# Kernel tuning notes

Measured on AMD Instinct MI355X. Metric: run time of the kernel, lower is better.

The kernel has to match this reference:

```python
import jax, jax.numpy as jnp
import numpy as np

NIN = 4096
NOUT = 4096
LN_EPS = 1e-5  # torch.nn.LayerNorm default


def setup_inputs() -> dict:
    key = jax.random.key(0)
    ks = jax.random.split(key, 8)
    x = jax.random.normal(ks[0], (1, NIN), dtype=jnp.float32)
    hid = jax.random.normal(ks[1], (1, NOUT), dtype=jnp.float32)
    hebb = jnp.zeros((NOUT, NOUT), dtype=jnp.float32) + 1e-6  # initialZeroHebb
    # parameters
    w_in = 0.01 * jax.random.normal(ks[2], (NOUT, NIN), dtype=jnp.float32)  # inp_lin weight (no bias)
    w = 0.01 * jnp.eye(NOUT, NOUT, dtype=jnp.float32)                        # Plastic.w
    alpha = 0.01 * jax.random.normal(ks[3], (NOUT, NOUT), dtype=jnp.float32)
    b = 0.01 * jax.random.normal(ks[4], (NOUT,), dtype=jnp.float32)
    lamda = 0.01 * jnp.ones((1,), dtype=jnp.float32)
    pred_eta = 0.01 * jax.random.normal(ks[5], (NOUT, NOUT), dtype=jnp.float32)
    pred_eta_b = 0.01 * jax.random.normal(ks[6], (NOUT,), dtype=jnp.float32)
    ln_gamma = jnp.ones((NOUT,), dtype=jnp.float32)
    ln_beta = jnp.zeros((NOUT,), dtype=jnp.float32)
    return {"x": x, "hid": hid, "hebb": hebb, "w_in": w_in, "w": w,
            "alpha": alpha, "b": b, "lamda": lamda, "pred_eta": pred_eta,
            "pred_eta_b": pred_eta_b, "ln_gamma": ln_gamma, "ln_beta": ln_beta}


def reference(x, hid, hebb, w_in, w, alpha, b, lamda, pred_eta, pred_eta_b, ln_gamma, ln_beta):
    # Cell.forward (nonlin = ReLU for both wx and the post-LN output)
    wx = jax.nn.relu(x @ w_in.T)                       # [1, nout]
    wh = hid @ (w + alpha * hebb) + b                  # Plastic.forward, [1, nout]
    s = wx + wh
    mu = jnp.mean(s, axis=-1, keepdims=True)
    var = jnp.mean((s - mu) ** 2, axis=-1, keepdims=True)
    ln = ln_gamma * (s - mu) * jax.lax.rsqrt(var + LN_EPS) + ln_beta
    wy = jax.nn.relu(ln)                               # new hidden state, [1, nout]
    # Plastic.update_hebb(x=hid, y=wh, hebb)
    eta_hat = jax.nn.sigmoid(wh @ pred_eta + pred_eta_b)           # [1, nout]
    outer = hid[0, :, None] * wh[0, None, :]                        # [nout, nout]
    hebb_new = (1.0 - lamda) * hebb + eta_hat.T * outer             # row i scaled by eta_hat[0, i]
    return wy, hebb_new
```

## Files before the change

### kernel.cpp

```cpp
#include <hip/hip_runtime.h>
#include <hip/hip_bf16.h>
#include <math.h>

#define N 4096
#define NGRP 16
#define NF4 (N * (N / 4))

typedef float f32x4 __attribute__((ext_vector_type(4)));

__inline__ __device__ float waveReduceSum(float v) {
    #pragma unroll
    for (int o = 32; o > 0; o >>= 1) v += __shfl_down(v, o);
    return v;
}

#define LD4(p, o) (*reinterpret_cast<const float4*>((p) + (o)))

__inline__ __device__ f32x4 ntld4(const float* p) {
    return __builtin_nontemporal_load(reinterpret_cast<const f32x4*>(p));
}

template<int ITERS>
__global__ __launch_bounds__(256) void k_sweep_wh_t(const float* __restrict__ hid,
                                                    const float* __restrict__ w,
                                                    const float* __restrict__ alpha,
                                                    const float* __restrict__ hebb,
                                                    float* __restrict__ part,
                                                    int G) {
    int b = blockIdx.x, t = threadIdx.x;
    int p = b >> 2;
    int j0 = (((b & 3) << 8) | t) * 4;
    int P = G >> 2;
    size_t step = (size_t)G * 1024;
    size_t off = (size_t)(((b << 8) | t)) * 4;

    f32x4 wv[ITERS], av[ITERS], bv[ITERS];
    float hv[ITERS];
    #pragma unroll
    for (int k = 0; k < ITERS; ++k) {
        size_t o = off + (size_t)k * step;
        wv[k] = ntld4(w + o);
        av[k] = ntld4(alpha + o);
        bv[k] = *reinterpret_cast<const f32x4*>(hebb + o);
    }
    #pragma unroll
    for (int k = 0; k < ITERS; ++k) hv[k] = hid[k * P + p];

    f32x4 acc = {0.f, 0.f, 0.f, 0.f};
    #pragma unroll
    for (int k = 0; k < ITERS; ++k) {
        float h = hv[k];
        acc.x = fmaf(h, fmaf(av[k].x, bv[k].x, wv[k].x), acc.x);
        acc.y = fmaf(h, fmaf(av[k].y, bv[k].y, wv[k].y), acc.y);
        acc.z = fmaf(h, fmaf(av[k].z, bv[k].z, wv[k].z), acc.z);
        acc.w = fmaf(h, fmaf(av[k].w, bv[k].w, wv[k].w), acc.w);
    }
    *reinterpret_cast<f32x4*>(part + (size_t)p * N + j0) = acc;
}

__global__ __launch_bounds__(256) void k_sweep_wh(const float* __restrict__ hid,
                                                  const float* __restrict__ w,
                                                  const float* __restrict__ alpha,
                                                  const float* __restrict__ hebb,
                                                  float* __restrict__ part,
                                                  int G, int iters) {
    int b = blockIdx.x, t = threadIdx.x;
    int p = b >> 2;
    int j0 = (((b & 3) << 8) | t) * 4;
    int P = G >> 2;
    float4 acc = make_float4(0.f, 0.f, 0.f, 0.f);
    size_t step = (size_t)G * 1024;
    size_t off = (size_t)(((b << 8) | t)) * 4;
    #pragma unroll 8
    for (int k = 0; k < iters; ++k, off += step) {
        float h = hid[k * P + p];
        float4 wv = LD4(w, off);
        float4 av = LD4(alpha, off);
        float4 hv = LD4(hebb, off);
        acc.x = fmaf(h, fmaf(av.x, hv.x, wv.x), acc.x);
        acc.y = fmaf(h, fmaf(av.y, hv.y, wv.y), acc.y);
        acc.z = fmaf(h, fmaf(av.z, hv.z, wv.z), acc.z);
        acc.w = fmaf(h, fmaf(av.w, hv.w, wv.w), acc.w);
    }
    *reinterpret_cast<float4*>(part + (size_t)p * N + j0) = acc;
}

__global__ __launch_bounds__(256) void k_sweep_eta(const float* __restrict__ wh,
                                                   const float* __restrict__ pe,
                                                   float* __restrict__ part,
                                                   int G, int iters) {
    int b = blockIdx.x, t = threadIdx.x;
    int p = b >> 2;
    int j0 = (((b & 3) << 8) | t) * 4;
    int P = G >> 2;
    float4 acc = make_float4(0.f, 0.f, 0.f, 0.f);
    size_t step = (size_t)G * 1024;
    size_t off = (size_t)(((b << 8) | t)) * 4;
    #pragma unroll 8
    for (int k = 0; k < iters; ++k, off += step) {
        float h = wh[k * P + p];
        float4 pv = LD4(pe, off);
        acc.x = fmaf(h, pv.x, acc.x);
        acc.y = fmaf(h, pv.y, acc.y);
        acc.z = fmaf(h, pv.z, acc.z);
        acc.w = fmaf(h, pv.w, acc.w);
    }
    *reinterpret_cast<float4*>(part + (size_t)p * N + j0) = acc;
}

__global__ __launch_bounds__(256) void k_sweep_wx(const float* __restrict__ x,
                                                  const float* __restrict__ w_in,
                                                  float* __restrict__ part_wx,
                                                  int G, int iters) {
    __shared__ float red[4];
    int b = blockIdx.x, t = threadIdx.x;
    int p = b >> 2;
    int P = G >> 2;
    int j0 = (((b & 3) << 8) | t) * 4;
    float4 xv = LD4(x, j0);
    size_t step = (size_t)G * 1024;
    size_t off = (size_t)(((b << 8) | t)) * 4;
    int wid = t >> 6, lane = t & 63;
    for (int k = 0; k < iters; ++k, off += step) {
        float4 wv = LD4(w_in, off);
        float d = wv.x * xv.x + wv.y * xv.y + wv.z * xv.z + wv.w * xv.w;
        d = waveReduceSum(d);
        if (lane == 0) red[wid] = d;
        __syncthreads();
        if (t == 0)
            part_wx[(size_t)(b & 3) * N + (k * P + p)] = red[0] + red[1] + red[2] + red[3];
        __syncthreads();
    }
}

__global__ __launch_bounds__(256) void k_red(const float* __restrict__ part,
                                             float* __restrict__ part2,
                                             int cpg) {
    int g  = blockIdx.y;
    int j0 = (blockIdx.x * 256 + threadIdx.x) * 4;
    const float4* p4 = reinterpret_cast<const float4*>(part);
    float4 s = make_float4(0.f, 0.f, 0.f, 0.f);
    #pragma unroll 8
    for (int c = 0; c < cpg; ++c) {
        float4 v = p4[((size_t)(g * cpg + c) * N + j0) >> 2];
        s.x += v.x; s.y += v.y; s.z += v.z; s.w += v.w;
    }
    *reinterpret_cast<float4*>(part2 + (size_t)g * N + j0) = s;
}

__global__ __launch_bounds__(1024) void k_ln(const float* __restrict__ part2,
                                             const float* __restrict__ part_wx,
                                             const float* __restrict__ b,
                                             const float* __restrict__ gamma,
                                             const float* __restrict__ beta,
                                             float* __restrict__ wh_out,
                                             float* __restrict__ wy_out) {
    __shared__ float red[16];
    __shared__ float bc[2];
    int tid = threadIdx.x;
    int wid = tid >> 6, lane = tid & 63;
    float sv[4];
    float lsum = 0.f;
    #pragma unroll
    for (int q = 0; q < 4; ++q) {
        int j = q * 1024 + tid;
        float acc = b[j];
        #pragma unroll
        for (int g = 0; g < NGRP; ++g) acc += part2[(size_t)g * N + j];
        wh_out[j] = acc;
        float wx = part_wx[j] + part_wx[N + j] + part_wx[2 * N + j] + part_wx[3 * N + j];
        float s = acc + fmaxf(wx, 0.f);
        sv[q] = s;
        lsum += s;
    }
    float wv = waveReduceSum(lsum);
    if (lane == 0) red[wid] = wv;
    __syncthreads();
    if (tid < 64) {
        float t = (tid < 16) ? red[tid] : 0.f;
        t = waveReduceSum(t);
        if (tid == 0) bc[0] = t * (1.f / N);
    }
    __syncthreads();
    float mean = bc[0];
    __syncthreads();
    float lsq = 0.f;
    #pragma unroll
    for (int q = 0; q < 4; ++q) { float d = sv[q] - mean; lsq += d * d; }
    wv = waveReduceSum(lsq);
    if (lane == 0) red[wid] = wv;
    __syncthreads();
    if (tid < 64) {
        float t = (tid < 16) ? red[tid] : 0.f;
        t = waveReduceSum(t);
        if (tid == 0) bc[1] = t * (1.f / N);
    }
    __syncthreads();
    float rstd = rsqrtf(bc[1] + 1e-5f);
    #pragma unroll
    for (int q = 0; q < 4; ++q) {
        int j = q * 1024 + tid;
        float ln = fmaf(gamma[j] * (sv[q] - mean), rstd, beta[j]);
        wy_out[j] = fmaxf(ln, 0.f);
    }
}

__global__ __launch_bounds__(256) void k_eta_fin(const float* __restrict__ part2,
                                                 const float* __restrict__ pb,
                                                 float* __restrict__ eta) {
    int j0 = (blockIdx.x * 256 + threadIdx.x) * 4;
    float4 s = *reinterpret_cast<const float4*>(pb + j0);
    #pragma unroll
    for (int g = 0; g < NGRP; ++g) {
        float4 v = *reinterpret_cast<const float4*>(part2 + (size_t)g * N + j0);
        s.x += v.x; s.y += v.y; s.z += v.z; s.w += v.w;
    }
    float4 r;
    r.x = 1.f / (1.f + expf(-s.x));
    r.y = 1.f / (1.f + expf(-s.y));
    r.z = 1.f / (1.f + expf(-s.z));
    r.w = 1.f / (1.f + expf(-s.w));
    *reinterpret_cast<float4*>(eta + j0) = r;
}

__global__ __launch_bounds__(256) void k_hebb(const float* __restrict__ hebb,
                                              const float* __restrict__ eta,
                                              const float* __restrict__ hid,
                                              const float* __restrict__ wh,
                                              const float* __restrict__ lamda,
                                              float* __restrict__ out,
                                              int G, int iters) {
    int b = blockIdx.x, t = threadIdx.x;
    int p = b >> 2;
    int P = G >> 2;
    int j0 = (((b & 3) << 8) | t) * 4;
    float decay = 1.f - lamda[0];
    float4 w4 = LD4(wh, j0);
    size_t step = (size_t)G * 1024;
    size_t off = (size_t)(((b << 8) | t)) * 4;
    #pragma unroll 4
    for (int k = 0; k < iters; ++k, off += step) {
        int i = k * P + p;
        float coef = eta[i] * hid[i];
        float4 h = LD4(hebb, off);
        f32x4 r;
        r.x = fmaf(decay, h.x, coef * w4.x);
        r.y = fmaf(decay, h.y, coef * w4.y);
        r.z = fmaf(decay, h.z, coef * w4.z);
        r.w = fmaf(decay, h.w, coef * w4.w);
        __builtin_nontemporal_store(r, reinterpret_cast<f32x4*>(out + off));
    }
}

extern "C" void kernel_launch(void* const* d_in, const int* in_sizes, int n_in,
                              void* d_out, int out_size, void* d_ws, size_t ws_size,
                              hipStream_t stream) {
    const float* x         = (const float*)d_in[0];
    const float* hid       = (const float*)d_in[1];
    const float* hebb      = (const float*)d_in[2];
    const float* w_in      = (const float*)d_in[3];
    const float* w         = (const float*)d_in[4];
    const float* alpha     = (const float*)d_in[5];
    const float* b         = (const float*)d_in[6];
    const float* lamda     = (const float*)d_in[7];
    const float* pred_eta  = (const float*)d_in[8];
    const float* pred_eta_b= (const float*)d_in[9];
    const float* ln_gamma  = (const float*)d_in[10];
    const float* ln_beta   = (const float*)d_in[11];

    float* wy       = (float*)d_out;
    float* hebb_out = (float*)d_out + N;

    int G = 2048;
    if ((ws_size / 4) < ((size_t)(G / 4) * N + (NGRP + 6) * N)) G = 512;
    int P = G / 4;
    int iters = NF4 / (G * 256);
    int cpg = P / NGRP;

    float* ws      = (float*)d_ws;
    float* part    = ws;
    float* part2   = part + (size_t)P * N;
    float* part_wx = part2 + (size_t)NGRP * N;
    float* wh      = part_wx + 4 * N;
    float* eta     = wh + N;

    if (G == 2048) {
        k_sweep_wh_t<8><<<G, 256, 0, stream>>>(hid, w, alpha, hebb, part, G);
    } else {
        k_sweep_wh<<<G, 256, 0, stream>>>(hid, w, alpha, hebb, part, G, iters);
    }
    k_sweep_wx <<<G, 256, 0, stream>>>(x, w_in, part_wx, G, iters);
    k_red      <<<dim3(4, NGRP), 256, 0, stream>>>(part, part2, cpg);
    k_ln       <<<1, 1024, 0, stream>>>(part2, part_wx, b, ln_gamma, ln_beta, wh, wy);
    k_sweep_eta<<<G, 256, 0, stream>>>(wh, pred_eta, part, G, iters);
    k_red      <<<dim3(4, NGRP), 256, 0, stream>>>(part, part2, cpg);
    k_eta_fin  <<<4, 256, 0, stream>>>(part2, pred_eta_b, eta);
    k_hebb     <<<G, 256, 0, stream>>>(hebb, eta, hid, wh, lamda, hebb_out, G, iters);
}
```

Baseline: 101.3 us.

## Fuse wx GEMV into reduction kernel and batch pred_eta sweep loads

Replaces the strided per-iteration-synchronized wx sweep with a row-per-block GEMV that is merged into the first partial-sum reduction launch. Each block reads one contiguous w_in row with nontemporal loads and applies ReLU directly, which removes the per-iteration block barriers and one launch. Adds a templated eta sweep that issues all pred_eta loads up front for more memory-level parallelism, and raises the hebb unroll factor. The risk is imbalance: the 4096 GEMV blocks and 64 reduction blocks now share one grid.

```diff
diff --git a/kernel.cpp b/kernel.cpp
--- a/kernel.cpp
+++ b/kernel.cpp
@@ -4,7 +4,6 @@
 
 #define N 4096
 #define NGRP 16
-#define NF4 (N * (N / 4))
 
 typedef float f32x4 __attribute__((ext_vector_type(4)));
 
@@ -85,6 +84,37 @@
     *reinterpret_cast<float4*>(part + (size_t)p * N + j0) = acc;
 }
 
+template<int ITERS>
+__global__ __launch_bounds__(256) void k_sweep_eta_t(const float* __restrict__ wh,
+                                                     const float* __restrict__ pe,
+                                                     float* __restrict__ part,
+                                                     int G) {
+    int b = blockIdx.x, t = threadIdx.x;
+    int p = b >> 2;
+    int j0 = (((b & 3) << 8) | t) * 4;
+    int P = G >> 2;
+    size_t step = (size_t)G * 1024;
+    size_t off = (size_t)(((b << 8) | t)) * 4;
+
+    f32x4 pv[ITERS];
+    float hv[ITERS];
+    #pragma unroll
+    for (int k = 0; k < ITERS; ++k) pv[k] = ntld4(pe + off + (size_t)k * step);
+    #pragma unroll
+    for (int k = 0; k < ITERS; ++k) hv[k] = wh[k * P + p];
+
+    f32x4 acc = {0.f, 0.f, 0.f, 0.f};
+    #pragma unroll
+    for (int k = 0; k < ITERS; ++k) {
+        float h = hv[k];
+        acc.x = fmaf(h, pv[k].x, acc.x);
+        acc.y = fmaf(h, pv[k].y, acc.y);
+        acc.z = fmaf(h, pv[k].z, acc.z);
+        acc.w = fmaf(h, pv[k].w, acc.w);
+    }
+    *reinterpret_cast<f32x4*>(part + (size_t)p * N + j0) = acc;
+}
+
 __global__ __launch_bounds__(256) void k_sweep_eta(const float* __restrict__ wh,
                                                    const float* __restrict__ pe,
                                                    float* __restrict__ part,
@@ -108,28 +138,44 @@
     *reinterpret_cast<float4*>(part + (size_t)p * N + j0) = acc;
 }
 
-__global__ __launch_bounds__(256) void k_sweep_wx(const float* __restrict__ x,
-                                                  const float* __restrict__ w_in,
-                                                  float* __restrict__ part_wx,
-                                                  int G, int iters) {
-    __shared__ float red[4];
-    int b = blockIdx.x, t = threadIdx.x;
-    int p = b >> 2;
-    int P = G >> 2;
-    int j0 = (((b & 3) << 8) | t) * 4;
-    float4 xv = LD4(x, j0);
-    size_t step = (size_t)G * 1024;
-    size_t off = (size_t)(((b << 8) | t)) * 4;
-    int wid = t >> 6, lane = t & 63;
-    for (int k = 0; k < iters; ++k, off += step) {
-        float4 wv = LD4(w_in, off);
-        float d = wv.x * xv.x + wv.y * xv.y + wv.z * xv.z + wv.w * xv.w;
-        d = waveReduceSum(d);
-        if (lane == 0) red[wid] = d;
+__global__ __launch_bounds__(256) void k_red_wx(const float* __restrict__ part,
+                                                float* __restrict__ part2,
+                                                int cpg,
+                                                const float* __restrict__ x,
+                                                const float* __restrict__ w_in,
+                                                float* __restrict__ wx_out,
+                                                int nred) {
+    int t = threadIdx.x;
+    if ((int)blockIdx.x < nred) {
+        int g  = blockIdx.x >> 2;
+        int xt = blockIdx.x & 3;
+        int j0 = (xt * 256 + t) * 4;
+        const float4* p4 = reinterpret_cast<const float4*>(part);
+        float4 s = make_float4(0.f, 0.f, 0.f, 0.f);
+        #pragma unroll 8
+        for (int c = 0; c < cpg; ++c) {
+            float4 v = p4[((size_t)(g * cpg + c) * N + j0) >> 2];
+            s.x += v.x; s.y += v.y; s.z += v.z; s.w += v.w;
+        }
+        *reinterpret_cast<float4*>(part2 + (size_t)g * N + j0) = s;
+    } else {
+        int j = blockIdx.x - nred;
+        const float* row = w_in + (size_t)j * N;
+        const float4* xv = reinterpret_cast<const float4*>(x);
+        float sum = 0.f;
+        #pragma unroll
+        for (int k = t; k < N / 4; k += 256) {
+            f32x4 a = ntld4(row + k * 4);
+            float4 c = xv[k];
+            sum += a.x * c.x + a.y * c.y + a.z * c.z + a.w * c.w;
+        }
+        sum = waveReduceSum(sum);
+        __shared__ float wsum[4];
+        int wid = t >> 6, lane = t & 63;
+        if (lane == 0) wsum[wid] = sum;
         __syncthreads();
         if (t == 0)
-            part_wx[(size_t)(b & 3) * N + (k * P + p)] = red[0] + red[1] + red[2] + red[3];
-        __syncthreads();
+            wx_out[j] = fmaxf(wsum[0] + wsum[1] + wsum[2] + wsum[3], 0.f);
     }
 }
 
@@ -149,7 +195,7 @@
 }
 
 __global__ __launch_bounds__(1024) void k_ln(const float* __restrict__ part2,
-                                             const float* __restrict__ part_wx,
+                                             const float* __restrict__ wx,
                                              const float* __restrict__ b,
                                              const float* __restrict__ gamma,
                                              const float* __restrict__ beta,
@@ -168,8 +214,7 @@
         #pragma unroll
         for (int g = 0; g < NGRP; ++g) acc += part2[(size_t)g * N + j];
         wh_out[j] = acc;
-        float wx = part_wx[j] + part_wx[N + j] + part_wx[2 * N + j] + part_wx[3 * N + j];
-        float s = acc + fmaxf(wx, 0.f);
+        float s = acc + wx[j];
         sv[q] = s;
         lsum += s;
     }
@@ -238,7 +283,7 @@
     float4 w4 = LD4(wh, j0);
     size_t step = (size_t)G * 1024;
     size_t off = (size_t)(((b << 8) | t)) * 4;
-    #pragma unroll 4
+    #pragma unroll 8
     for (int k = 0; k < iters; ++k, off += step) {
         int i = k * P + p;
         float coef = eta[i] * hid[i];
@@ -272,28 +317,32 @@
     float* hebb_out = (float*)d_out + N;
 
     int G = 2048;
-    if ((ws_size / 4) < ((size_t)(G / 4) * N + (NGRP + 6) * N)) G = 512;
+    if ((ws_size / 4) < ((size_t)(G / 4) * N + (NGRP + 3) * (size_t)N)) G = 512;
     int P = G / 4;
-    int iters = NF4 / (G * 256);
     int cpg = P / NGRP;
-
-    float* ws      = (float*)d_ws;
-    float* part    = ws;
-    float* part2   = part + (size_t)P * N;
-    float* part_wx = part2 + (size_t)NGRP * N;
-    float* wh      = part_wx + 4 * N;
-    float* eta     = wh + N;
+    int iters = (N * (N / 4)) / (G * 256);
+    int nred = 4 * NGRP;
+
+    float* ws    = (float*)d_ws;
+    float* part  = ws;
+    float* part2 = part + (size_t)P * N;
+    float* wx    = part2 + (size_t)NGRP * N;
+    float* wh    = wx + N;
+    float* eta   = wh + N;
 
     if (G == 2048) {
         k_sweep_wh_t<8><<<G, 256, 0, stream>>>(hid, w, alpha, hebb, part, G);
     } else {
         k_sweep_wh<<<G, 256, 0, stream>>>(hid, w, alpha, hebb, part, G, iters);
     }
-    k_sweep_wx <<<G, 256, 0, stream>>>(x, w_in, part_wx, G, iters);
-    k_red      <<<dim3(4, NGRP), 256, 0, stream>>>(part, part2, cpg);
-    k_ln       <<<1, 1024, 0, stream>>>(part2, part_wx, b, ln_gamma, ln_beta, wh, wy);
-    k_sweep_eta<<<G, 256, 0, stream>>>(wh, pred_eta, part, G, iters);
-    k_red      <<<dim3(4, NGRP), 256, 0, stream>>>(part, part2, cpg);
-    k_eta_fin  <<<4, 256, 0, stream>>>(part2, pred_eta_b, eta);
-    k_hebb     <<<G, 256, 0, stream>>>(hebb, eta, hid, wh, lamda, hebb_out, G, iters);
-}
+    k_red_wx <<<nred + N, 256, 0, stream>>>(part, part2, cpg, x, w_in, wx, nred);
+    k_ln     <<<1, 1024, 0, stream>>>(part2, wx, b, ln_gamma, ln_beta, wh, wy);
+    if (G == 2048) {
+        k_sweep_eta_t<8><<<G, 256, 0, stream>>>(wh, pred_eta, part, G);
+    } else {
+        k_sweep_eta<<<G, 256, 0, stream>>>(wh, pred_eta, part, G, iters);
+    }
+    k_red    <<<dim3(4, NGRP), 256, 0, stream>>>(part, part2, cpg);
+    k_eta_fin<<<4, 256, 0, stream>>>(part2, pred_eta_b, eta);
+    k_hebb   <<<G, 256, 0, stream>>>(hebb, eta, hid, wh, lamda, hebb_out, G, iters);
+}
```

New measurement: 107.4 us. +6.1%, slower.
